# Optimization experiments

Hardware: AMD Instinct MI355X
Metric: run time of the kernel (lower is better)

## Reference

```python
import jax, jax.numpy as jnp
import numpy as np

EPS = 1e-5

def _ln(x, g=None, b=None):
    m = x.mean(-1, keepdims=True)
    v = x.var(-1, keepdims=True)
    y = (x - m) / jnp.sqrt(v + EPS)
    if g is not None:
        y = y * g + b
    return y

def setup_inputs() -> dict:
    B, N, D, E, NC = 32, 256, 1024, 4096, 16
    key = jax.random.key(0)
    ks = iter(jax.random.split(key, 24))
    def rn(shape, s=0.02):
        return jax.random.normal(next(ks), shape, jnp.float32) * s
    return dict(
        h=jax.random.normal(next(ks), (B, N, D), jnp.float32),
        Wpp=rn((D, E)), bpp=jnp.zeros(E), Wsp=rn((D, E)), bsp=jnp.zeros(E),
        Wq=rn((E, E)), bq=jnp.zeros(E),
        Wk=rn((E, E)), bk=jnp.zeros(E),
        Wv=rn((E, E)), bv=jnp.zeros(E),
        g_pfs=jnp.ones(D + E), b_pfs=jnp.zeros(D + E),
        Wpfs=rn((D + E, D)), bpfs=jnp.zeros(D),
        g_sfs=jnp.ones(E), b_sfs=jnp.zeros(E),
        Wsfs=rn((E, D)), bsfs=jnp.zeros(D),
        Wpc=rn((D, NC)), bpc=jnp.zeros(NC),
        Wc0=rn((NC, 8, D)), bc0=jnp.zeros((NC, 8)),
        Wc1=rn((NC, 16, D)), bc1=jnp.zeros((NC, 16)),
        Wc2=rn((NC, 32, D)), bc2=jnp.zeros((NC, 32)),
    )

def reference(h, Wpp, bpp, Wsp, bsp, Wq, bq, Wk, bk, Wv, bv,
              g_pfs, b_pfs, Wpfs, bpfs, g_sfs, b_sfs, Wsfs, bsfs,
              Wpc, bpc, Wc0, bc0, Wc1, bc1, Wc2, bc2):
    B, N, D = h.shape
    H = 4
    E = Wpp.shape[1]
    hd = E // H
    scale = hd ** -0.5
    gelu = lambda x: jax.nn.gelu(x, approximate=False)  # torch exact GELU
    pp = gelu(h @ Wpp + bpp)                  # [B,N,E]
    sp = gelu(h @ Wsp + bsp)                  # [B,N,E]
    Q = (pp @ Wq + bq).reshape(B, N, H, hd)
    K = (sp @ Wk + bk).reshape(B, N, H, hd)
    V = (sp @ Wv + bv).reshape(B, N, H, hd)
    attn = jax.nn.softmax(jnp.einsum('bqhd,bkhd->bhqk', Q, K) * scale, axis=-1)
    intf = jnp.einsum('bhqk,bkhd->bqhd', attn, V).reshape(B, N, E)
    intf = _ln(intf)                          # F.layer_norm, no affine
    pvec = _ln((_ln(jnp.concatenate([h, intf], -1), g_pfs, b_pfs) @ Wpfs + bpfs).mean(1))  # [B,D]
    svec = _ln((_ln(sp, g_sfs, b_sfs) @ Wsfs + bsfs).mean(1))                               # [B,D]
    parent_logits = pvec @ Wpc + bpc          # [B,NC]
    y_hat = jnp.argmax(parent_logits, axis=1) # argmax(softmax) == argmax(logits)
    # routed child heads: gather per-sample weight by parent argmax, batched matvec
    child = tuple(
        jnp.einsum('bd,bnd->bn', svec, W[y_hat]) + b[y_hat]
        for W, b in ((Wc0, bc0), (Wc1, bc1), (Wc2, bc2))
    )
    return (parent_logits,) + child + (pvec, svec)
```

## Files before the change

### kernel.cpp

```cpp
#include <hip/hip_runtime.h>
#include <hip/hip_bf16.h>

typedef __bf16 bf16x8 __attribute__((ext_vector_type(8)));
typedef float f32x4 __attribute__((ext_vector_type(4)));
typedef unsigned long long u64;

#define EPSV 1e-5f

__device__ __forceinline__ float bf2f(unsigned short u){
  unsigned int x = ((unsigned int)u) << 16;
  return __builtin_bit_cast(float, x);
}
__device__ __forceinline__ unsigned short f2bf(float f){
  __bf16 b = (__bf16)f;
  return __builtin_bit_cast(unsigned short, b);
}
__device__ __forceinline__ float gelu_exact(float x){
  return 0.5f * x * (1.0f + erff(x * 0.7071067811865476f));
}
__device__ __forceinline__ void gload_lds16(const void* g, void* l){
  __builtin_amdgcn_global_load_lds((const __attribute__((address_space(1))) unsigned int*)g,
                                   (__attribute__((address_space(3))) unsigned int*)l, 16, 0, 0);
}

struct GemmCore {
  char* smem; int t, w, l, wm, wn, lr, lg, bm0, bn0, nk;
  int srow, sslot;
  const unsigned short *A, *B; int lda, ldb;
  f32x4 acc[8][4];
  bf16x8 a0[4][2], a1[4][2], b0[2][2], b1[2][2];

  __device__ __forceinline__ void stage(int kt, int mat, int hf, int q){
    if (kt >= nk) return;
    const int r_h = q*64 + srow;
    const int s_ = sslot ^ ((r_h >> 1) & 7);
    const unsigned short* gp = (mat ? B + (size_t)(bn0 + hf*128 + r_h)*ldb
                                    : A + (size_t)(bm0 + hf*128 + r_h)*lda)
                               + (kt << 6) + s_*8;
    char* lp = smem + mat*65536 + (kt&1)*32768 + hf*16384 + q*8192 + t*16;
    gload_lds16((const void*)gp, (void*)lp);
  }
  __device__ __forceinline__ bf16x8 rdA(int d, int fm, int kk){
    const int r = fm*16 + lr;
    const int s_ = (kk*4 + lg) ^ ((r >> 1) & 7);
    return *(const bf16x8*)(smem + d*32768 + wm*16384 + r*128 + s_*16);
  }
  __device__ __forceinline__ bf16x8 rdB(int d, int fn, int kk){
    const int r = (wn&1)*64 + fn*16 + lr;
    const int s_ = (kk*4 + lg) ^ ((r >> 1) & 7);
    return *(const bf16x8*)(smem + 65536 + d*32768 + (wn>>1)*16384 + r*128 + s_*16);
  }
  __device__ __forceinline__ void ktile(int kt, int d){
    stage(kt+1, 0, 0, 1); stage(kt+1, 0, 1, 1);
    #pragma unroll
    for (int fm=0; fm<4; ++fm){ a0[fm][0] = rdA(d, fm, 0); a0[fm][1] = rdA(d, fm, 1); }
    #pragma unroll
    for (int fn=0; fn<2; ++fn){ b0[fn][0] = rdB(d, fn, 0); b0[fn][1] = rdB(d, fn, 1); }
    __builtin_amdgcn_s_barrier();
    __builtin_amdgcn_s_setprio(1);
    #pragma unroll
    for (int fm=0; fm<4; ++fm)
      #pragma unroll
      for (int fn=0; fn<2; ++fn)
        #pragma unroll
        for (int kk=0; kk<2; ++kk)
          acc[fm][fn] = __builtin_amdgcn_mfma_f32_16x16x32_bf16(a0[fm][kk], b0[fn][kk], acc[fm][fn], 0,0,0);
    __builtin_amdgcn_s_setprio(0);
    #pragma unroll
    for (int fn=0; fn<2; ++fn){ b1[fn][0] = rdB(d, fn+2, 0); b1[fn][1] = rdB(d, fn+2, 1); }
    __builtin_amdgcn_s_barrier();
    __builtin_amdgcn_s_setprio(1);
    #pragma unroll
    for (int fm=0; fm<4; ++fm)
      #pragma unroll
      for (int fn=0; fn<2; ++fn)
        #pragma unroll
        for (int kk=0; kk<2; ++kk)
          acc[fm][fn+2] = __builtin_amdgcn_mfma_f32_16x16x32_bf16(a0[fm][kk], b1[fn][kk], acc[fm][fn+2], 0,0,0);
    __builtin_amdgcn_s_setprio(0);
    stage(kt+2, 0, 0, 0); stage(kt+2, 0, 1, 0);
    stage(kt+2, 1, 0, 0); stage(kt+2, 1, 1, 0);
    #pragma unroll
    for (int fm=0; fm<4; ++fm){ a1[fm][0] = rdA(d, fm+4, 0); a1[fm][1] = rdA(d, fm+4, 1); }
    __builtin_amdgcn_s_barrier();
    __builtin_amdgcn_s_setprio(1);
    #pragma unroll
    for (int fm=0; fm<4; ++fm)
      #pragma unroll
      for (int fn=0; fn<2; ++fn)
        #pragma unroll
        for (int kk=0; kk<2; ++kk)
          acc[fm+4][fn+2] = __builtin_amdgcn_mfma_f32_16x16x32_bf16(a1[fm][kk], b1[fn][kk], acc[fm+4][fn+2], 0,0,0);
    __builtin_amdgcn_s_setprio(0);
    stage(kt+2, 1, 0, 1); stage(kt+2, 1, 1, 1);
    __builtin_amdgcn_s_barrier();
    __builtin_amdgcn_s_setprio(1);
    #pragma unroll
    for (int fm=0; fm<4; ++fm)
      #pragma unroll
      for (int fn=0; fn<2; ++fn)
        #pragma unroll
        for (int kk=0; kk<2; ++kk)
          acc[fm+4][fn] = __builtin_amdgcn_mfma_f32_16x16x32_bf16(a1[fm][kk], b0[fn][kk], acc[fm+4][fn], 0,0,0);
    __builtin_amdgcn_s_setprio(0);
    if (kt + 2 < nk) { asm volatile("s_waitcnt vmcnt(6)" ::: "memory"); }
    else             { asm volatile("s_waitcnt vmcnt(0)" ::: "memory"); }
  }
  __device__ __forceinline__ void run(){
    #pragma unroll
    for (int i=0;i<8;++i)
      #pragma unroll
      for (int j=0;j<4;++j){ f32x4 zz = {0.f,0.f,0.f,0.f}; acc[i][j] = zz; }
    stage(0,0,0,0); stage(0,0,1,0); stage(0,0,0,1); stage(0,0,1,1);
    stage(0,1,0,0); stage(0,1,1,0); stage(0,1,0,1); stage(0,1,1,1);
    stage(1,0,0,0); stage(1,0,1,0);
    stage(1,1,0,0); stage(1,1,1,0);
    stage(1,1,0,1); stage(1,1,1,1);
    asm volatile("s_waitcnt vmcnt(6)" ::: "memory");
    __builtin_amdgcn_s_barrier();
    for (int kt = 0; kt < nk; kt += 2){ ktile(kt, 0); ktile(kt+1, 1); }
  }
  __device__ __forceinline__ void init(char* sm, int Kd, const unsigned short* A_,
                                       const unsigned short* B_, int lda_, int ldb_,
                                       int bm0_, int bn0_){
    smem = sm; t = threadIdx.x; w = t>>6; l = t&63;
    wm = w>>2; wn = w&3; lr = l&15; lg = l>>4;
    srow = t>>3; sslot = t&7;
    A = A_; B = B_; lda = lda_; ldb = ldb_; bm0 = bm0_; bn0 = bn0_;
    nk = Kd >> 6;
  }
};

template<int MODE>
__global__ __launch_bounds__(512, 2)
void gemm256(const unsigned short* __restrict__ A, const unsigned short* __restrict__ B,
             const float* __restrict__ bias0, const float* __restrict__ bias1,
             void* __restrict__ C0v, void* __restrict__ C1v,
             int Kd, int lda, int ldb, int ldc)
{
  __shared__ char smem[131072];
  const int nbx = gridDim.x;
  const int nwg = nbx * gridDim.y;
  int bid = blockIdx.y*nbx + blockIdx.x;
  if ((nwg & 7) == 0) bid = (bid & 7)*(nwg >> 3) + (bid >> 3);
  GemmCore g;
  g.init(smem, Kd, A, B, lda, ldb, (bid / nbx) * 256, (bid % nbx) * 256);
  g.run();
  #pragma unroll
  for (int fm=0; fm<8; ++fm){
    #pragma unroll
    for (int fn=0; fn<4; ++fn){
      const int row0 = g.bm0 + g.wm*128 + fm*16 + g.lg*4;
      const int col  = g.bn0 + g.wn*64 + fn*16 + g.lr;
      f32x4 v = g.acc[fm][fn];
      if constexpr (MODE == 3){
        unsigned short* C = (unsigned short*)C0v;
        const float bb = bias0[col];
        u64 pack = 0;
        #pragma unroll
        for (int j=0;j<4;++j) pack |= (u64)f2bf(v[j] + bb) << (16*j);
        *(u64*)(C + (size_t)col*256 + (size_t)(row0>>8)*1048576 + (row0&255)) = pack;
      } else {
        const bool hi = (MODE == 0) && (col >= 4096);
        unsigned short* C = (unsigned short*)(hi ? C1v : C0v);
        const int c2 = hi ? (col - 4096) : col;
        const float bb = hi ? bias1[c2] : bias0[c2];
        #pragma unroll
        for (int j=0;j<4;++j){
          float x = v[j] + bb;
          if constexpr (MODE==0) x = gelu_exact(x);
          C[(size_t)(row0+j)*ldc + c2] = f2bf(x);
        }
      }
    }
  }
}

__global__ __launch_bounds__(512, 2)
void gemm_qkv(const unsigned short* __restrict__ App, const unsigned short* __restrict__ Asp,
              const unsigned short* __restrict__ Wqkv,
              const float* __restrict__ bq, const float* __restrict__ bk,
              const float* __restrict__ bv,
              unsigned short* __restrict__ Qo, unsigned short* __restrict__ Ko,
              unsigned short* __restrict__ Vto)
{
  __shared__ char smem[131072];
  const int z = blockIdx.z;
  const int nbx = gridDim.x;
  const int nwg = nbx * gridDim.y;
  int bid = blockIdx.y*nbx + blockIdx.x;
  if ((nwg & 7) == 0) bid = (bid & 7)*(nwg >> 3) + (bid >> 3);
  GemmCore g;
  g.init(smem, 4096, (z==0) ? App : Asp, Wqkv + (size_t)z*16777216, 4096, 4096,
         (bid / nbx) * 256, (bid % nbx) * 256);
  g.run();
  const float* bias = (z==0) ? bq : (z==1) ? bk : bv;
  #pragma unroll
  for (int fm=0; fm<8; ++fm){
    #pragma unroll
    for (int fn=0; fn<4; ++fn){
      const int row0 = g.bm0 + g.wm*128 + fm*16 + g.lg*4;
      const int col  = g.bn0 + g.wn*64 + fn*16 + g.lr;
      f32x4 v = g.acc[fm][fn];
      const float bb = bias[col];
      if (z == 2){
        u64 pack = 0;
        #pragma unroll
        for (int j=0;j<4;++j) pack |= (u64)f2bf(v[j] + bb) << (16*j);
        *(u64*)(Vto + (size_t)col*256 + (size_t)(row0>>8)*1048576 + (row0&255)) = pack;
      } else {
        unsigned short* C = (z==0) ? Qo : Ko;
        #pragma unroll
        for (int j=0;j<4;++j) C[(size_t)(row0+j)*4096 + col] = f2bf(v[j] + bb);
      }
    }
  }
}

template<int MODE>
__global__ __launch_bounds__(256)
void gemm_bt(const unsigned short* __restrict__ A, const unsigned short* __restrict__ B,
             const float* __restrict__ bias, void* __restrict__ Cv,
             int Kd, int lda, int ldb, int ldc,
             long sA2, long sA1, long sB2, long sB1, long sC2, long sC1,
             float scale)
{
  __shared__ unsigned short lds[2][2][4096];
  const int t = threadIdx.x;
  const int w = t >> 6, l = t & 63;
  const int z = blockIdx.z;
  A += (size_t)(z>>2)*sA2 + (size_t)(z&3)*sA1;
  B += (size_t)(z>>2)*sB2 + (size_t)(z&3)*sB1;
  const int bm0 = blockIdx.y * 128, bn0 = blockIdx.x * 128;
  const int nk = Kd >> 5;

  const int sr = l >> 2;
  const int ss = l & 3;

  f32x4 acc[4][4];
  #pragma unroll
  for (int i=0;i<4;++i){
    #pragma unroll
    for (int j=0;j<4;++j){ f32x4 zz = {0.f,0.f,0.f,0.f}; acc[i][j] = zz; }
  }

  const int wm = w >> 1, wn = w & 1;
  const int lr = l & 15, lg = l >> 4;

  auto stage = [&](int kt, int bb){
    const int k0 = kt << 5;
    #pragma unroll
    for (int i=0;i<2;++i){
      const int r  = w*32 + i*16 + sr;
      const int sa = ss ^ ((r>>1)&3);
      const unsigned short* ga = A + (size_t)(bm0 + r)*lda + (k0 + sa*8);
      gload_lds16((const void*)ga, (void*)((char*)&lds[bb][0][0] + w*2048 + i*1024));
      const unsigned short* gb = B + (size_t)(bn0 + r)*ldb + (k0 + sa*8);
      gload_lds16((const void*)gb, (void*)((char*)&lds[bb][1][0] + w*2048 + i*1024));
    }
  };

  int buf = 0;
  stage(0, 0);
  for (int kt=0; kt<nk; ++kt){
    __syncthreads();
    if (kt+1 < nk) stage(kt+1, buf^1);
    bf16x8 av[4], bv[4];
    #pragma unroll
    for (int fm=0; fm<4; ++fm){
      const int row = wm*64 + fm*16 + lr;
      const int sl  = lg ^ ((row>>1)&3);
      av[fm] = *(const bf16x8*)((const char*)&lds[buf][0][0] + row*64 + sl*16);
    }
    #pragma unroll
    for (int fn=0; fn<4; ++fn){
      const int col = wn*64 + fn*16 + lr;
      const int sl  = lg ^ ((col>>1)&3);
      bv[fn] = *(const bf16x8*)((const char*)&lds[buf][1][0] + col*64 + sl*16);
    }
    #pragma unroll
    for (int fm=0; fm<4; ++fm){
      #pragma unroll
      for (int fn=0; fn<4; ++fn)
        acc[fm][fn] = __builtin_amdgcn_mfma_f32_16x16x32_bf16(av[fm], bv[fn], acc[fm][fn], 0,0,0);
    }
    buf ^= 1;
  }

  const size_t coff = (size_t)(z>>2)*sC2 + (size_t)(z&3)*sC1;
  #pragma unroll
  for (int fm=0; fm<4; ++fm){
    #pragma unroll
    for (int fn=0; fn<4; ++fn){
      const int row0 = bm0 + wm*64 + fm*16 + lg*4;
      const int col  = bn0 + wn*64 + fn*16 + lr;
      f32x4 v = acc[fm][fn];
      if constexpr (MODE == 2){
        float* C = (float*)Cv + coff;
        #pragma unroll
        for (int j=0;j<4;++j) C[(size_t)(row0+j)*ldc + col] = v[j]*scale;
      }
    }
  }
}

__global__ __launch_bounds__(256)
void k_convh(const float* __restrict__ in, unsigned short* __restrict__ out){
  const size_t id = (size_t)blockIdx.x*256 + threadIdx.x;
  float4 v = ((const float4*)in)[id];
  u64 pack = (u64)f2bf(v.x) | ((u64)f2bf(v.y)<<16) | ((u64)f2bf(v.z)<<32) | ((u64)f2bf(v.w)<<48);
  *(u64*)(out + id*4) = pack;
}

__global__ __launch_bounds__(256)
void k_tconv3(const float* __restrict__ W0, const float* __restrict__ W1,
              const float* __restrict__ W2, unsigned short* __restrict__ Wt,
              int Kd, int N, long wtStride){
  __shared__ float lt[64][65];
  const int t = threadIdx.x;
  const int zz = blockIdx.z;
  const float* W = (zz==0) ? W0 : (zz==1) ? W1 : W2;
  unsigned short* Wtz = Wt + (size_t)zz * wtStride;
  const int n0 = blockIdx.x*64, k0 = blockIdx.y*64;
  #pragma unroll
  for (int i=0;i<16;++i){
    int lin = i*256 + t; int r = lin>>6, c = lin&63;
    lt[r][c] = W[(size_t)(k0+r)*N + n0 + c];
  }
  __syncthreads();
  #pragma unroll
  for (int i=0;i<16;++i){
    int lin = i*256 + t; int n = lin>>6, k = lin&63;
    Wtz[(size_t)(n0+n)*Kd + k0 + k] = f2bf(lt[k][n]);
  }
}

__global__ __launch_bounds__(256)
void k_tconv(const float* __restrict__ W, unsigned short* __restrict__ Wt, int Kd, int N){
  __shared__ float lt[64][65];
  const int t = threadIdx.x;
  const int n0 = blockIdx.x*64, k0 = blockIdx.y*64;
  #pragma unroll
  for (int i=0;i<16;++i){
    int lin = i*256 + t; int r = lin>>6, c = lin&63;
    lt[r][c] = W[(size_t)(k0+r)*N + n0 + c];
  }
  __syncthreads();
  #pragma unroll
  for (int i=0;i<16;++i){
    int lin = i*256 + t; int n = lin>>6, k = lin&63;
    Wt[(size_t)(n0+n)*Kd + k0 + k] = f2bf(lt[k][n]);
  }
}

__global__ __launch_bounds__(256)
void k_softmax(const float* __restrict__ S, unsigned short* __restrict__ P){
  const int t = threadIdx.x, w = t>>6, l = t&63;
  const size_t row = (size_t)blockIdx.x*4 + w;
  float4 v = *(const float4*)(S + row*256 + l*4);
  float m = fmaxf(fmaxf(v.x,v.y), fmaxf(v.z,v.w));
  #pragma unroll
  for (int off=32; off; off>>=1) m = fmaxf(m, __shfl_xor(m, off));
  float e0 = expf(v.x-m), e1 = expf(v.y-m), e2 = expf(v.z-m), e3 = expf(v.w-m);
  float s = e0+e1+e2+e3;
  #pragma unroll
  for (int off=32; off; off>>=1) s += __shfl_xor(s, off);
  const float inv = 1.0f/s;
  u64 pack = (u64)f2bf(e0*inv) | ((u64)f2bf(e1*inv)<<16) | ((u64)f2bf(e2*inv)<<32) | ((u64)f2bf(e3*inv)<<48);
  *(u64*)(P + row*256 + l*4) = pack;
}

__device__ __forceinline__ void blkred2(float& a, float& b, float* sred, int t){
  #pragma unroll
  for (int off=32; off; off>>=1){ a += __shfl_xor(a, off); b += __shfl_xor(b, off); }
  __syncthreads();
  if ((t&63)==0){ sred[(t>>6)*2] = a; sred[(t>>6)*2+1] = b; }
  __syncthreads();
  a = sred[0]+sred[2]+sred[4]+sred[6];
  b = sred[1]+sred[3]+sred[5]+sred[7];
}

__device__ __forceinline__ void blkred4(float& a, float& b, float& c, float& d,
                                        float* sred, int t){
  #pragma unroll
  for (int off=32; off; off>>=1){
    a += __shfl_xor(a, off); b += __shfl_xor(b, off);
    c += __shfl_xor(c, off); d += __shfl_xor(d, off);
  }
  __syncthreads();
  if ((t&63)==0){
    sred[(t>>6)*4]   = a; sred[(t>>6)*4+1] = b;
    sred[(t>>6)*4+2] = c; sred[(t>>6)*4+3] = d;
  }
  __syncthreads();
  a = sred[0]+sred[4]+sred[8]+sred[12];
  b = sred[1]+sred[5]+sred[9]+sred[13];
  c = sred[2]+sred[6]+sred[10]+sred[14];
  d = sred[3]+sred[7]+sred[11]+sred[15];
}

__global__ __launch_bounds__(256)
void k_stats(const float* __restrict__ h, const float* __restrict__ intf,
             const unsigned short* __restrict__ sp,
             const float* __restrict__ g_pfs, const float* __restrict__ b_pfs,
             const float* __restrict__ g_sfs, const float* __restrict__ b_sfs,
             float* __restrict__ part_p, float* __restrict__ part_s, int g0)
{
  __shared__ float sred[16];
  const int bl = blockIdx.x, grp = blockIdx.y, t = threadIdx.x;
  float zacc[20], wacc[16];
  #pragma unroll
  for (int j=0;j<20;++j) zacc[j]=0.f;
  #pragma unroll
  for (int j=0;j<16;++j) wacc[j]=0.f;
  for (int rr=0; rr<16; ++rr){
    const size_t r = (size_t)bl*256 + grp*16 + rr;
    float hv[4], iv[16], sv[16];
    #pragma unroll
    for (int j=0;j<4;++j) hv[j] = h[r*1024 + j*256 + t];
    float s1=0.f, s2=0.f;
    #pragma unroll
    for (int j=0;j<16;++j){ float x = intf[r*4096 + j*256 + t]; iv[j]=x; s1+=x; s2+=x*x; }
    float u1=0.f, u2=0.f;
    #pragma unroll
    for (int j=0;j<16;++j){ float x = bf2f(sp[r*4096 + j*256 + t]); sv[j]=x; u1+=x; u2+=x*x; }
    blkred4(s1,s2,u1,u2,sred,t);
    const float m1 = s1*(1.f/4096.f);
    const float rs1 = rsqrtf(fmaxf(s2*(1.f/4096.f) - m1*m1, 0.f) + EPSV);
    const float m3 = u1*(1.f/4096.f);
    const float rs3 = rsqrtf(fmaxf(u2*(1.f/4096.f) - m3*m3, 0.f) + EPSV);
    #pragma unroll
    for (int j=0;j<16;++j){ int idx = j*256+t; wacc[j] += ((sv[j]-m3)*rs3)*g_sfs[idx] + b_sfs[idx]; }
    float t1=0.f, t2=0.f;
    #pragma unroll
    for (int j=0;j<4;++j){ t1 += hv[j]; t2 += hv[j]*hv[j]; }
    #pragma unroll
    for (int j=0;j<16;++j){ float y = (iv[j]-m1)*rs1; iv[j]=y; t1+=y; t2+=y*y; }
    blkred2(t1,t2,sred,t);
    const float m2 = t1*(1.f/5120.f);
    const float rs2 = rsqrtf(fmaxf(t2*(1.f/5120.f) - m2*m2, 0.f) + EPSV);
    #pragma unroll
    for (int j=0;j<4;++j){ int idx = j*256+t; zacc[j] += ((hv[j]-m2)*rs2)*g_pfs[idx] + b_pfs[idx]; }
    #pragma unroll
    for (int j=0;j<16;++j){ int idx = 1024 + j*256+t; zacc[4+j] += ((iv[j]-m2)*rs2)*g_pfs[idx] + b_pfs[idx]; }
  }
  const size_t pb = (size_t)(g0 + bl)*16 + grp;
  #pragma unroll
  for (int j=0;j<20;++j) part_p[pb*5120 + j*256 + t] = zacc[j];
  #pragma unroll
  for (int j=0;j<16;++j) part_s[pb*4096 + j*256 + t] = wacc[j];
}

__global__ __launch_bounds__(256)
void k_reduce(const float* __restrict__ part_p, const float* __restrict__ part_s,
              float* __restrict__ xbar, float* __restrict__ ybar){
  int id = blockIdx.x*256 + threadIdx.x;
  if (id < 32*5120){
    const int b = id / 5120, i = id % 5120;
    float s = 0.f;
    for (int g=0; g<16; ++g) s += part_p[((size_t)b*16+g)*5120 + i];
    xbar[(size_t)b*5120 + i] = s * (1.f/256.f);
  } else {
    id -= 32*5120;
    const int b = id / 4096, i = id % 4096;
    float s = 0.f;
    for (int g=0; g<16; ++g) s += part_s[((size_t)b*16+g)*4096 + i];
    ybar[(size_t)b*4096 + i] = s * (1.f/256.f);
  }
}

__global__ __launch_bounds__(256)
void k_proj_part(const float* __restrict__ xbar, const float* __restrict__ ybar,
                 const float* __restrict__ Wpfs, const float* __restrict__ Wsfs,
                 float* __restrict__ pbuf){
  const int path = blockIdx.z;
  const int y = blockIdx.y;
  if (path == 1 && y >= 8) return;
  const int Kp = path ? 4096 : 5120;
  const float* X = path ? ybar : xbar;
  const float* W = path ? Wsfs : Wpfs;
  const int t = threadIdx.x;
  const int col = blockIdx.x*64 + (t & 63);
  const int sub = t >> 6;
  const int k0 = y*512 + sub*128;
  float acc[32];
  #pragma unroll
  for (int b=0;b<32;++b) acc[b] = 0.f;
  for (int i4=0; i4<32; ++i4){
    const int k = k0 + i4*4;
    float wv0 = W[(size_t)(k  )*1024 + col];
    float wv1 = W[(size_t)(k+1)*1024 + col];
    float wv2 = W[(size_t)(k+2)*1024 + col];
    float wv3 = W[(size_t)(k+3)*1024 + col];
    #pragma unroll
    for (int b=0;b<32;++b){
      float4 xv = *(const float4*)(X + (size_t)b*Kp + k);
      acc[b] += xv.x*wv0 + xv.y*wv1 + xv.z*wv2 + xv.w*wv3;
    }
  }
  float* dst = pbuf + ((size_t)(path*40 + y*4 + sub)*32)*1024 + col;
  #pragma unroll
  for (int b=0;b<32;++b) dst[(size_t)b*1024] = acc[b];
}

__global__ __launch_bounds__(256)
void k_projred(const float* __restrict__ pbuf,
               const float* __restrict__ bpfs, const float* __restrict__ bsfs,
               float* __restrict__ tpre, float* __restrict__ spre){
  const int id = blockIdx.x*256 + threadIdx.x;
  const int path = id >> 15;
  const int rem = id & 32767;
  const int b = rem >> 10, col = rem & 1023;
  const int ns = path ? 32 : 40;
  const float* src = pbuf + ((size_t)(path*40)*32 + b)*1024 + col;
  float s = path ? bsfs[col] : bpfs[col];
  for (int g=0; g<ns; ++g) s += src[(size_t)g*32*1024];
  (path ? spre : tpre)[(size_t)b*1024 + col] = s;
}

__global__ __launch_bounds__(256)
void k_lnrow(const float* __restrict__ tpre, const float* __restrict__ spre,
             float* __restrict__ out){
  __shared__ float sred[16];
  const int id = blockIdx.x, t = threadIdx.x;
  const int path = id >> 5, b = id & 31;
  const float* src = (path ? spre : tpre) + (size_t)b*1024;
  float v[4]; float s1=0.f, s2=0.f;
  #pragma unroll
  for (int j=0;j<4;++j){ v[j] = src[j*256+t]; s1 += v[j]; s2 += v[j]*v[j]; }
  blkred2(s1,s2,sred,t);
  const float m = s1*(1.f/1024.f);
  const float rs = rsqrtf(fmaxf(s2*(1.f/1024.f)-m*m,0.f)+EPSV);
  float* dst = out + (path ? 35072 : 2304) + (size_t)b*1024;
  #pragma unroll
  for (int j=0;j<4;++j) dst[j*256+t] = (v[j]-m)*rs;
}

__global__ __launch_bounds__(256)
void k_head(const float* __restrict__ Wpc, const float* __restrict__ bpc,
            const float* __restrict__ Wc0, const float* __restrict__ bc0,
            const float* __restrict__ Wc1, const float* __restrict__ bc1,
            const float* __restrict__ Wc2, const float* __restrict__ bc2,
            float* __restrict__ out){
  __shared__ float slog[16];
  __shared__ int sy;
  const int b = blockIdx.x, t = threadIdx.x, w = t>>6, l = t&63;
  const float* pv = out + 2304 + (size_t)b*1024;
  const float* sv = out + 35072 + (size_t)b*1024;
  #pragma unroll
  for (int jj=0; jj<4; ++jj){
    const int j = w*4 + jj;
    float a = 0.f;
    for (int i=l; i<1024; i+=64) a += pv[i]*Wpc[(size_t)i*16 + j];
    #pragma unroll
    for (int off=32; off; off>>=1) a += __shfl_xor(a, off);
    if (l==0){ const float lgv = a + bpc[j]; slog[j] = lgv; out[b*16 + j] = lgv; }
  }
  __syncthreads();
  if (t==0){
    int best=0; float bvv = slog[0];
    for (int i=1;i<16;++i) if (slog[i] > bvv){ bvv = slog[i]; best = i; }
    sy = best;
  }
  __syncthreads();
  const int y = sy;
  const float* Ws[3] = {Wc0, Wc1, Wc2};
  const float* bs[3] = {bc0, bc1, bc2};
  const int nouts[3] = {8,16,32};
  const int ooff[3]  = {512, 768, 1280};
  for (int hI=0; hI<3; ++hI){
    const int no = nouts[hI];
    for (int n = w; n < no; n += 4){
      const float* wr = Ws[hI] + ((size_t)y*no + n)*1024;
      float a = 0.f;
      for (int i=l; i<1024; i+=64) a += sv[i]*wr[i];
      #pragma unroll
      for (int off=32; off; off>>=1) a += __shfl_xor(a, off);
      if (l==0) out[ooff[hI] + b*no + n] = a + bs[hI][(size_t)y*no + n];
    }
  }
}

extern "C" void kernel_launch(void* const* d_in, const int* in_sizes, int n_in,
                              void* d_out, int out_size, void* d_ws, size_t ws_size,
                              hipStream_t stream)
{
  const float* h    = (const float*)d_in[0];
  const float* Wpp  = (const float*)d_in[1];
  const float* bpp  = (const float*)d_in[2];
  const float* Wsp  = (const float*)d_in[3];
  const float* bsp  = (const float*)d_in[4];
  const float* Wq   = (const float*)d_in[5];
  const float* bq   = (const float*)d_in[6];
  const float* Wk   = (const float*)d_in[7];
  const float* bk   = (const float*)d_in[8];
  const float* Wv   = (const float*)d_in[9];
  const float* bv   = (const float*)d_in[10];
  const float* g_pfs= (const float*)d_in[11];
  const float* b_pfs= (const float*)d_in[12];
  const float* Wpfs = (const float*)d_in[13];
  const float* bpfs = (const float*)d_in[14];
  const float* g_sfs= (const float*)d_in[15];
  const float* b_sfs= (const float*)d_in[16];
  const float* Wsfs = (const float*)d_in[17];
  const float* bsfs = (const float*)d_in[18];
  const float* Wpc  = (const float*)d_in[19];
  const float* bpc  = (const float*)d_in[20];
  const float* Wc0  = (const float*)d_in[21];
  const float* bc0  = (const float*)d_in[22];
  const float* Wc1  = (const float*)d_in[23];
  const float* bc1  = (const float*)d_in[24];
  const float* Wc2  = (const float*)d_in[25];
  const float* bc2  = (const float*)d_in[26];
  float* out = (float*)d_out;
  char* ws = (char*)d_ws;
  (void)in_sizes; (void)n_in; (void)out_size;

  struct PlanT { int G, NS, hoist; };
  const PlanT plans[8] = {{16,4096,2},{16,4096,1},{16,4096,0},{8,4096,0},{4,4096,0},{2,4096,0},{1,4096,0},{1,1024,0}};
  int G = 0, NS = 0, HOIST = 0;
  size_t oWt=0,oWps=0,oWq=0,oSP=0;
  size_t oPp=0,oPs=0,oXb=0,oYb=0,oTp=0,oSp=0,oPbf=0,oHb=0,oPb=0,oSb=0,oQ=0,oK=0,oVt=0;
  for (int pi = 0; pi < 8; ++pi){
    const size_t g = plans[pi].G, ns = plans[pi].NS;
    const int hoist = plans[pi].hoist;
    size_t off = 0;
    auto alloc = [&](size_t bytes){ size_t o = off; off += (bytes + 255) & ~255ULL; return o; };
    size_t wt=0, wps=0, wq=0, sp2=0, pbf=0, hb=0, pb=0;
    size_t pp_, ps_, xb, yb, tp, sp_, sb, q, k, vt;
    if (hoist >= 1){
      wps = alloc(8192ULL*1024*2);
      wq  = alloc(3*4096ULL*4096*2);
      pp_ = alloc(32ULL*16*5120*4);
      ps_ = alloc(32ULL*16*4096*4);
      xb = alloc(32*5120*4); yb = alloc(32*4096*4);
      tp = alloc(32*1024*4); sp_ = alloc(32*1024*4);
      sb = alloc(g*2097152);
      q  = alloc(g*2097152);
      k  = alloc(g*2097152);
      vt = alloc(g*2097152);
      if (hoist == 2){
        sp2 = alloc(g*2097152);
        pb = sp2;
      } else {
        sp2 = alloc(g*1572864);
        pb = k;
      }
      pbf = q; hb = vt;
    } else {
      wt = alloc(ns*4096*2);
      pp_ = alloc(32ULL*16*5120*4);
      ps_ = alloc(32ULL*16*4096*4);
      xb = alloc(32*5120*4); yb = alloc(32*4096*4);
      tp = alloc(32*1024*4); sp_ = alloc(32*1024*4);
      pbf = alloc(2*40*32*1024*4);
      hb = alloc(g*524288);
      pb = alloc(g*2097152);
      sb = alloc(g*2097152);
      q  = alloc(g*2097152);
      k  = alloc(g*2097152);
      vt = alloc(g*2097152);
      sp2 = pb;
    }
    if (off <= ws_size){
      G = (int)g; NS = (int)ns; HOIST = hoist;
      oWt=wt; oWps=wps; oWq=wq; oSP=sp2;
      oPp=pp_; oPs=ps_; oXb=xb; oYb=yb; oTp=tp; oSp=sp_; oPbf=pbf;
      oHb=hb; oPb=pb; oSb=sb; oQ=q; oK=k; oVt=vt;
      break;
    }
  }
  if (!G) return;

  unsigned short* Wt    = (unsigned short*)(ws + oWt);
  unsigned short* WpsT  = (unsigned short*)(ws + oWps);
  unsigned short* WqkvT = (unsigned short*)(ws + oWq);
  float* part_p = (float*)(ws + oPp);
  float* part_s = (float*)(ws + oPs);
  float* xbar   = (float*)(ws + oXb);
  float* ybar   = (float*)(ws + oYb);
  float* tpre   = (float*)(ws + oTp);
  float* spre   = (float*)(ws + oSp);
  float* pbuf   = (float*)(ws + oPbf);
  unsigned short* h_bf = (unsigned short*)(ws + oHb);
  unsigned short* pp   = (unsigned short*)(ws + oPb);
  unsigned short* sp   = (unsigned short*)(ws + oSb);
  unsigned short* Q    = (unsigned short*)(ws + oQ);
  unsigned short* Kb   = (unsigned short*)(ws + oK);
  unsigned short* Vt   = (unsigned short*)(ws + oVt);
  float*          S    = (float*)(ws + oSP);
  unsigned short* P    = (unsigned short*)(ws + oSP + (size_t)G*1048576);
  float*          intf = (float*)(ws + oQ);

  const float scale = 1.0f/32.0f;
  (void)oK;

  if (HOIST >= 1){
    hipLaunchKernelGGL(k_tconv, dim3(64,16), dim3(256), 0, stream, Wpp, WpsT, 1024, 4096);
    hipLaunchKernelGGL(k_tconv, dim3(64,16), dim3(256), 0, stream, Wsp, WpsT + 4096ULL*1024, 1024, 4096);
    hipLaunchKernelGGL(k_tconv3, dim3(64,64,3), dim3(256), 0, stream,
                       Wq, Wk, Wv, WqkvT, 4096, 4096, 16777216L);
  }

  for (int g0 = 0; g0 < 32; g0 += G){
    const float* h_g = h + (size_t)g0*262144;

    hipLaunchKernelGGL(k_convh, dim3(G*256), dim3(256), 0, stream, h_g, h_bf);

    if (HOIST == 2){
      hipLaunchKernelGGL(gemm256<0>, dim3(32,G), dim3(512), 0, stream,
                         h_bf, WpsT, bpp, bsp, (void*)pp, (void*)sp, 1024, 1024,1024,4096);
      hipLaunchKernelGGL(gemm_qkv, dim3(16,G,3), dim3(512), 0, stream,
                         pp, sp, WqkvT, bq, bk, bv, Q, Kb, Vt);
    } else if (HOIST == 1){
      hipLaunchKernelGGL(gemm256<0>, dim3(32,G), dim3(512), 0, stream,
                         h_bf, WpsT, bpp, bsp, (void*)pp, (void*)sp, 1024, 1024,1024,4096);
      hipLaunchKernelGGL(gemm256<1>, dim3(16,G), dim3(512), 0, stream,
                         pp, WqkvT, bq, bq, (void*)Q, (void*)Q, 4096, 4096,4096,4096);
      hipLaunchKernelGGL(gemm256<1>, dim3(16,G), dim3(512), 0, stream,
                         sp, WqkvT + 16777216ULL, bk, bk, (void*)Kb, (void*)Kb, 4096, 4096,4096,4096);
      hipLaunchKernelGGL(gemm256<3>, dim3(16,G), dim3(512), 0, stream,
                         sp, WqkvT + 33554432ULL, bv, bv, (void*)Vt, (void*)Vt, 4096, 4096,4096,256);
    } else {
      hipLaunchKernelGGL(k_tconv, dim3(64,16), dim3(256), 0, stream, Wpp, Wt, 1024, 4096);
      hipLaunchKernelGGL(gemm256<0>, dim3(16,G), dim3(512), 0, stream,
                         h_bf, Wt, bpp, bpp, (void*)pp, (void*)pp, 1024, 1024,1024,4096);
      for (int nso = 0; nso < 4096; nso += NS){
        hipLaunchKernelGGL(k_tconv, dim3(NS/64,64), dim3(256), 0, stream, Wq + nso, Wt, 4096, 4096);
        hipLaunchKernelGGL(gemm256<1>, dim3(NS/256,G), dim3(512), 0, stream,
                           pp, Wt, bq + nso, bq + nso, (void*)(Q + nso), (void*)(Q + nso), 4096, 4096,4096,4096);
      }
      hipLaunchKernelGGL(k_tconv, dim3(64,16), dim3(256), 0, stream, Wsp, Wt, 1024, 4096);
      hipLaunchKernelGGL(gemm256<0>, dim3(16,G), dim3(512), 0, stream,
                         h_bf, Wt, bsp, bsp, (void*)sp, (void*)sp, 1024, 1024,1024,4096);
      for (int nso = 0; nso < 4096; nso += NS){
        hipLaunchKernelGGL(k_tconv, dim3(NS/64,64), dim3(256), 0, stream, Wk + nso, Wt, 4096, 4096);
        hipLaunchKernelGGL(gemm256<1>, dim3(NS/256,G), dim3(512), 0, stream,
                           sp, Wt, bk + nso, bk + nso, (void*)(Kb + nso), (void*)(Kb + nso), 4096, 4096,4096,4096);
      }
      for (int nso = 0; nso < 4096; nso += NS){
        hipLaunchKernelGGL(k_tconv, dim3(NS/64,64), dim3(256), 0, stream, Wv + nso, Wt, 4096, 4096);
        hipLaunchKernelGGL(gemm256<3>, dim3(NS/256,G), dim3(512), 0, stream,
                           sp, Wt, bv + nso, bv + nso, (void*)(Vt + (size_t)nso*256), (void*)(Vt + (size_t)nso*256), 4096, 4096,4096,256);
      }
    }
    hipLaunchKernelGGL(gemm_bt<2>, dim3(2,2,G*4), dim3(256), 0, stream,
                       Q, Kb, (const float*)nullptr, (void*)S, 1024, 4096,4096,256,
                       1048576L,1024L, 1048576L,1024L, 262144L,65536L, scale);
    hipLaunchKernelGGL(k_softmax, dim3(G*256), dim3(256), 0, stream, S, P);
    hipLaunchKernelGGL(gemm_bt<2>, dim3(8,2,G*4), dim3(256), 0, stream,
                       P, Vt, (const float*)nullptr, (void*)intf, 256, 256,256,4096,
                       262144L,65536L, 1048576L,262144L, 1048576L,1024L, 1.f);
    hipLaunchKernelGGL(k_stats, dim3(G,16), dim3(256), 0, stream,
                       h_g, intf, sp, g_pfs, b_pfs, g_sfs, b_sfs, part_p, part_s, g0);
  }

  hipLaunchKernelGGL(k_reduce, dim3(1152), dim3(256), 0, stream, part_p, part_s, xbar, ybar);
  hipLaunchKernelGGL(k_proj_part, dim3(16,10,2), dim3(256), 0, stream,
                     xbar, ybar, Wpfs, Wsfs, pbuf);
  hipLaunchKernelGGL(k_projred, dim3(256), dim3(256), 0, stream,
                     pbuf, bpfs, bsfs, tpre, spre);
  hipLaunchKernelGGL(k_lnrow, dim3(64), dim3(256), 0, stream, tpre, spre, out);
  hipLaunchKernelGGL(k_head, dim3(32), dim3(256), 0, stream,
                     Wpc, bpc, Wc0, bc0, Wc1, bc1, Wc2, bc2, out);
}
```

Baseline: 1.281 ms.

## Add aliased single-pass workspace plan and store attention output in bf16

Adds a primary path that processes the whole batch at once using a compact workspace. Buffers are aliased between stages (pp/Vt, Q/intf, h_bf/Kb/pbuf, S/part_p) and one transposed weight buffer is reused for Wq, Wk and Wv, so the grouped loop and its extra launches go away when the workspace fits. The attention-output GEMM now writes intf as bf16 (new MODE 5) and k_stats reads it as bf16, which halves that traffic but lowers the precision of the layer-norm input. The fallback plan list is reduced and the weight-streaming variants are removed.

```diff
diff --git a/kernel.cpp b/kernel.cpp
--- a/kernel.cpp
+++ b/kernel.cpp
@@ -299,6 +299,10 @@
         float* C = (float*)Cv + coff;
         #pragma unroll
         for (int j=0;j<4;++j) C[(size_t)(row0+j)*ldc + col] = v[j]*scale;
+      } else if constexpr (MODE == 5){
+        unsigned short* C = (unsigned short*)Cv + coff;
+        #pragma unroll
+        for (int j=0;j<4;++j) C[(size_t)(row0+j)*ldc + col] = f2bf(v[j]*scale);
       }
     }
   }
@@ -310,6 +314,24 @@
   float4 v = ((const float4*)in)[id];
   u64 pack = (u64)f2bf(v.x) | ((u64)f2bf(v.y)<<16) | ((u64)f2bf(v.z)<<32) | ((u64)f2bf(v.w)<<48);
   *(u64*)(out + id*4) = pack;
+}
+
+__global__ __launch_bounds__(256)
+void k_tconv(const float* __restrict__ W, unsigned short* __restrict__ Wt, int Kd, int N){
+  __shared__ float lt[64][65];
+  const int t = threadIdx.x;
+  const int n0 = blockIdx.x*64, k0 = blockIdx.y*64;
+  #pragma unroll
+  for (int i=0;i<16;++i){
+    int lin = i*256 + t; int r = lin>>6, c = lin&63;
+    lt[r][c] = W[(size_t)(k0+r)*N + n0 + c];
+  }
+  __syncthreads();
+  #pragma unroll
+  for (int i=0;i<16;++i){
+    int lin = i*256 + t; int n = lin>>6, k = lin&63;
+    Wt[(size_t)(n0+n)*Kd + k0 + k] = f2bf(lt[k][n]);
+  }
 }
 
 __global__ __launch_bounds__(256)
@@ -336,24 +358,6 @@
 }
 
 __global__ __launch_bounds__(256)
-void k_tconv(const float* __restrict__ W, unsigned short* __restrict__ Wt, int Kd, int N){
-  __shared__ float lt[64][65];
-  const int t = threadIdx.x;
-  const int n0 = blockIdx.x*64, k0 = blockIdx.y*64;
-  #pragma unroll
-  for (int i=0;i<16;++i){
-    int lin = i*256 + t; int r = lin>>6, c = lin&63;
-    lt[r][c] = W[(size_t)(k0+r)*N + n0 + c];
-  }
-  __syncthreads();
-  #pragma unroll
-  for (int i=0;i<16;++i){
-    int lin = i*256 + t; int n = lin>>6, k = lin&63;
-    Wt[(size_t)(n0+n)*Kd + k0 + k] = f2bf(lt[k][n]);
-  }
-}
-
-__global__ __launch_bounds__(256)
 void k_softmax(const float* __restrict__ S, unsigned short* __restrict__ P){
   const int t = threadIdx.x, w = t>>6, l = t&63;
   const size_t row = (size_t)blockIdx.x*4 + w;
@@ -400,7 +404,7 @@
 }
 
 __global__ __launch_bounds__(256)
-void k_stats(const float* __restrict__ h, const float* __restrict__ intf,
+void k_stats(const float* __restrict__ h, const unsigned short* __restrict__ intf,
              const unsigned short* __restrict__ sp,
              const float* __restrict__ g_pfs, const float* __restrict__ b_pfs,
              const float* __restrict__ g_sfs, const float* __restrict__ b_sfs,
@@ -420,7 +424,7 @@
     for (int j=0;j<4;++j) hv[j] = h[r*1024 + j*256 + t];
     float s1=0.f, s2=0.f;
     #pragma unroll
-    for (int j=0;j<16;++j){ float x = intf[r*4096 + j*256 + t]; iv[j]=x; s1+=x; s2+=x*x; }
+    for (int j=0;j<16;++j){ float x = bf2f(intf[r*4096 + j*256 + t]); iv[j]=x; s1+=x; s2+=x*x; }
     float u1=0.f, u2=0.f;
     #pragma unroll
     for (int j=0;j<16;++j){ float x = bf2f(sp[r*4096 + j*256 + t]); sv[j]=x; u1+=x; u2+=x*x; }
@@ -616,63 +620,109 @@
   char* ws = (char*)d_ws;
   (void)in_sizes; (void)n_in; (void)out_size;
 
-  struct PlanT { int G, NS, hoist; };
-  const PlanT plans[8] = {{16,4096,2},{16,4096,1},{16,4096,0},{8,4096,0},{4,4096,0},{2,4096,0},{1,4096,0},{1,1024,0}};
-  int G = 0, NS = 0, HOIST = 0;
-  size_t oWt=0,oWps=0,oWq=0,oSP=0;
+  const float scale = 1.0f/32.0f;
+
+  {
+    size_t off = 0;
+    auto alloc = [&](size_t bytes){ size_t o = off; off += (bytes + 255) & ~255ULL; return o; };
+    size_t oWps = alloc(8192ULL*1024*2);
+    size_t oWb  = alloc(4096ULL*4096*2);
+    size_t oA   = alloc(64ULL<<20);
+    size_t oB   = alloc(64ULL<<20);
+    size_t oC   = alloc(64ULL<<20);
+    size_t oD   = alloc(64ULL<<20);
+    size_t oXb  = alloc(32*5120*4);
+    size_t oYb  = alloc(32*4096*4);
+    size_t oTp  = alloc(32*1024*4);
+    size_t oSp  = alloc(32*1024*4);
+    if (off <= ws_size){
+      unsigned short* WpsT = (unsigned short*)(ws + oWps);
+      unsigned short* wbuf = (unsigned short*)(ws + oWb);
+      unsigned short* pp   = (unsigned short*)(ws + oA);
+      unsigned short* Vt   = (unsigned short*)(ws + oA);
+      unsigned short* sp   = (unsigned short*)(ws + oB);
+      unsigned short* Q    = (unsigned short*)(ws + oC);
+      unsigned short* intf = (unsigned short*)(ws + oC);
+      unsigned short* h_bf = (unsigned short*)(ws + oD);
+      unsigned short* Kb   = (unsigned short*)(ws + oD);
+      float* pbuf   = (float*)(ws + oD);
+      float* S      = (float*)(ws + oWb);
+      unsigned short* P = (unsigned short*)(ws + oWps);
+      float* part_p = (float*)(ws + oWb);
+      float* part_s = (float*)(ws + oWb + ((32ULL*16*5120*4 + 255) & ~255ULL));
+      float* xbar   = (float*)(ws + oXb);
+      float* ybar   = (float*)(ws + oYb);
+      float* tpre   = (float*)(ws + oTp);
+      float* spre   = (float*)(ws + oSp);
+
+      hipLaunchKernelGGL(k_tconv, dim3(64,16), dim3(256), 0, stream, Wpp, WpsT, 1024, 4096);
+      hipLaunchKernelGGL(k_tconv, dim3(64,16), dim3(256), 0, stream, Wsp, WpsT + 4096ULL*1024, 1024, 4096);
+      hipLaunchKernelGGL(k_convh, dim3(8192), dim3(256), 0, stream, h, h_bf);
+      hipLaunchKernelGGL(gemm256<0>, dim3(32,32), dim3(512), 0, stream,
+                         h_bf, WpsT, bpp, bsp, (void*)pp, (void*)sp, 1024, 1024,1024,4096);
+      hipLaunchKernelGGL(k_tconv, dim3(64,64), dim3(256), 0, stream, Wq, wbuf, 4096, 4096);
+      hipLaunchKernelGGL(gemm256<1>, dim3(16,32), dim3(512), 0, stream,
+                         pp, wbuf, bq, bq, (void*)Q, (void*)Q, 4096, 4096,4096,4096);
+      hipLaunchKernelGGL(k_tconv, dim3(64,64), dim3(256), 0, stream, Wk, wbuf, 4096, 4096);
+      hipLaunchKernelGGL(gemm256<1>, dim3(16,32), dim3(512), 0, stream,
+                         sp, wbuf, bk, bk, (void*)Kb, (void*)Kb, 4096, 4096,4096,4096);
+      hipLaunchKernelGGL(k_tconv, dim3(64,64), dim3(256), 0, stream, Wv, wbuf, 4096, 4096);
+      hipLaunchKernelGGL(gemm256<3>, dim3(16,32), dim3(512), 0, stream,
+                         sp, wbuf, bv, bv, (void*)Vt, (void*)Vt, 4096, 4096,4096,256);
+      hipLaunchKernelGGL(gemm_bt<2>, dim3(2,2,128), dim3(256), 0, stream,
+                         Q, Kb, (const float*)nullptr, (void*)S, 1024, 4096,4096,256,
+                         1048576L,1024L, 1048576L,1024L, 262144L,65536L, scale);
+      hipLaunchKernelGGL(k_softmax, dim3(8192), dim3(256), 0, stream, S, P);
+      hipLaunchKernelGGL(gemm_bt<5>, dim3(8,2,128), dim3(256), 0, stream,
+                         P, Vt, (const float*)nullptr, (void*)intf, 256, 256,256,4096,
+                         262144L,65536L, 1048576L,262144L, 1048576L,1024L, 1.f);
+      hipLaunchKernelGGL(k_stats, dim3(32,16), dim3(256), 0, stream,
+                         h, intf, sp, g_pfs, b_pfs, g_sfs, b_sfs, part_p, part_s, 0);
+      hipLaunchKernelGGL(k_reduce, dim3(1152), dim3(256), 0, stream, part_p, part_s, xbar, ybar);
+      hipLaunchKernelGGL(k_proj_part, dim3(16,10,2), dim3(256), 0, stream,
+                         xbar, ybar, Wpfs, Wsfs, pbuf);
+      hipLaunchKernelGGL(k_projred, dim3(256), dim3(256), 0, stream,
+                         pbuf, bpfs, bsfs, tpre, spre);
+      hipLaunchKernelGGL(k_lnrow, dim3(64), dim3(256), 0, stream, tpre, spre, out);
+      hipLaunchKernelGGL(k_head, dim3(32), dim3(256), 0, stream,
+                         Wpc, bpc, Wc0, bc0, Wc1, bc1, Wc2, bc2, out);
+      return;
+    }
+  }
+
+  struct PlanT { int G, hoist; };
+  const PlanT plans[3] = {{16,2},{16,1},{8,1}};
+  int G = 0, HOIST = 0;
+  size_t oWps=0,oWq=0,oSP=0;
   size_t oPp=0,oPs=0,oXb=0,oYb=0,oTp=0,oSp=0,oPbf=0,oHb=0,oPb=0,oSb=0,oQ=0,oK=0,oVt=0;
-  for (int pi = 0; pi < 8; ++pi){
-    const size_t g = plans[pi].G, ns = plans[pi].NS;
+  for (int pi = 0; pi < 3; ++pi){
+    const size_t g = plans[pi].G;
     const int hoist = plans[pi].hoist;
     size_t off = 0;
     auto alloc = [&](size_t bytes){ size_t o = off; off += (bytes + 255) & ~255ULL; return o; };
-    size_t wt=0, wps=0, wq=0, sp2=0, pbf=0, hb=0, pb=0;
-    size_t pp_, ps_, xb, yb, tp, sp_, sb, q, k, vt;
-    if (hoist >= 1){
-      wps = alloc(8192ULL*1024*2);
-      wq  = alloc(3*4096ULL*4096*2);
-      pp_ = alloc(32ULL*16*5120*4);
-      ps_ = alloc(32ULL*16*4096*4);
-      xb = alloc(32*5120*4); yb = alloc(32*4096*4);
-      tp = alloc(32*1024*4); sp_ = alloc(32*1024*4);
-      sb = alloc(g*2097152);
-      q  = alloc(g*2097152);
-      k  = alloc(g*2097152);
-      vt = alloc(g*2097152);
-      if (hoist == 2){
-        sp2 = alloc(g*2097152);
-        pb = sp2;
-      } else {
-        sp2 = alloc(g*1572864);
-        pb = k;
-      }
-      pbf = q; hb = vt;
-    } else {
-      wt = alloc(ns*4096*2);
-      pp_ = alloc(32ULL*16*5120*4);
-      ps_ = alloc(32ULL*16*4096*4);
-      xb = alloc(32*5120*4); yb = alloc(32*4096*4);
-      tp = alloc(32*1024*4); sp_ = alloc(32*1024*4);
-      pbf = alloc(2*40*32*1024*4);
-      hb = alloc(g*524288);
-      pb = alloc(g*2097152);
-      sb = alloc(g*2097152);
-      q  = alloc(g*2097152);
-      k  = alloc(g*2097152);
-      vt = alloc(g*2097152);
-      sp2 = pb;
-    }
+    size_t wps = alloc(8192ULL*1024*2);
+    size_t wq  = alloc(3*4096ULL*4096*2);
+    size_t pp_ = alloc(32ULL*16*5120*4);
+    size_t ps_ = alloc(32ULL*16*4096*4);
+    size_t xb = alloc(32*5120*4); size_t yb = alloc(32*4096*4);
+    size_t tp = alloc(32*1024*4); size_t sp_ = alloc(32*1024*4);
+    size_t sb = alloc(g*2097152);
+    size_t q  = alloc(g*2097152);
+    size_t k  = alloc(g*2097152);
+    size_t vt = alloc(g*2097152);
+    size_t sp2, pb;
+    if (hoist == 2){ sp2 = alloc(g*2097152); pb = sp2; }
+    else           { sp2 = alloc(g*1572864); pb = k; }
     if (off <= ws_size){
-      G = (int)g; NS = (int)ns; HOIST = hoist;
-      oWt=wt; oWps=wps; oWq=wq; oSP=sp2;
-      oPp=pp_; oPs=ps_; oXb=xb; oYb=yb; oTp=tp; oSp=sp_; oPbf=pbf;
-      oHb=hb; oPb=pb; oSb=sb; oQ=q; oK=k; oVt=vt;
+      G = (int)g; HOIST = hoist;
+      oWps=wps; oWq=wq; oSP=sp2;
+      oPp=pp_; oPs=ps_; oXb=xb; oYb=yb; oTp=tp; oSp=sp_; oPbf=q;
+      oHb=vt; oPb=pb; oSb=sb; oQ=q; oK=k; oVt=vt;
       break;
     }
   }
   if (!G) return;
 
-  unsigned short* Wt    = (unsigned short*)(ws + oWt);
   unsigned short* WpsT  = (unsigned short*)(ws + oWps);
   unsigned short* WqkvT = (unsigned short*)(ws + oWq);
   float* part_p = (float*)(ws + oPp);
@@ -690,65 +740,34 @@
   unsigned short* Vt   = (unsigned short*)(ws + oVt);
   float*          S    = (float*)(ws + oSP);
   unsigned short* P    = (unsigned short*)(ws + oSP + (size_t)G*1048576);
-  float*          intf = (float*)(ws + oQ);
-
-  const float scale = 1.0f/32.0f;
-  (void)oK;
-
-  if (HOIST >= 1){
-    hipLaunchKernelGGL(k_tconv, dim3(64,16), dim3(256), 0, stream, Wpp, WpsT, 1024, 4096);
-    hipLaunchKernelGGL(k_tconv, dim3(64,16), dim3(256), 0, stream, Wsp, WpsT + 4096ULL*1024, 1024, 4096);
-    hipLaunchKernelGGL(k_tconv3, dim3(64,64,3), dim3(256), 0, stream,
-                       Wq, Wk, Wv, WqkvT, 4096, 4096, 16777216L);
-  }
+  unsigned short* intf = (unsigned short*)(ws + oQ);
+
+  hipLaunchKernelGGL(k_tconv, dim3(64,16), dim3(256), 0, stream, Wpp, WpsT, 1024, 4096);
+  hipLaunchKernelGGL(k_tconv, dim3(64,16), dim3(256), 0, stream, Wsp, WpsT + 4096ULL*1024, 1024, 4096);
+  hipLaunchKernelGGL(k_tconv3, dim3(64,64,3), dim3(256), 0, stream,
+                     Wq, Wk, Wv, WqkvT, 4096, 4096, 16777216L);
 
   for (int g0 = 0; g0 < 32; g0 += G){
     const float* h_g = h + (size_t)g0*262144;
-
     hipLaunchKernelGGL(k_convh, dim3(G*256), dim3(256), 0, stream, h_g, h_bf);
-
+    hipLaunchKernelGGL(gemm256<0>, dim3(32,G), dim3(512), 0, stream,
+                       h_bf, WpsT, bpp, bsp, (void*)pp, (void*)sp, 1024, 1024,1024,4096);
     if (HOIST == 2){
-      hipLaunchKernelGGL(gemm256<0>, dim3(32,G), dim3(512), 0, stream,
-                         h_bf, WpsT, bpp, bsp, (void*)pp, (void*)sp, 1024, 1024,1024,4096);
       hipLaunchKernelGGL(gemm_qkv, dim3(16,G,3), dim3(512), 0, stream,
                          pp, sp, WqkvT, bq, bk, bv, Q, Kb, Vt);
-    } else if (HOIST == 1){
-      hipLaunchKernelGGL(gemm256<0>, dim3(32,G), dim3(512), 0, stream,
-                         h_bf, WpsT, bpp, bsp, (void*)pp, (void*)sp, 1024, 1024,1024,4096);
+    } else {
       hipLaunchKernelGGL(gemm256<1>, dim3(16,G), dim3(512), 0, stream,
                          pp, WqkvT, bq, bq, (void*)Q, (void*)Q, 4096, 4096,4096,4096);
       hipLaunchKernelGGL(gemm256<1>, dim3(16,G), dim3(512), 0, stream,
                          sp, WqkvT + 16777216ULL, bk, bk, (void*)Kb, (void*)Kb, 4096, 4096,4096,4096);
       hipLaunchKernelGGL(gemm256<3>, dim3(16,G), dim3(512), 0, stream,
                          sp, WqkvT + 33554432ULL, bv, bv, (void*)Vt, (void*)Vt, 4096, 4096,4096,256);
-    } else {
-      hipLaunchKernelGGL(k_tconv, dim3(64,16), dim3(256), 0, stream, Wpp, Wt, 1024, 4096);
-      hipLaunchKernelGGL(gemm256<0>, dim3(16,G), dim3(512), 0, stream,
-                         h_bf, Wt, bpp, bpp, (void*)pp, (void*)pp, 1024, 1024,1024,4096);
-      for (int nso = 0; nso < 4096; nso += NS){
-        hipLaunchKernelGGL(k_tconv, dim3(NS/64,64), dim3(256), 0, stream, Wq + nso, Wt, 4096, 4096);
-        hipLaunchKernelGGL(gemm256<1>, dim3(NS/256,G), dim3(512), 0, stream,
-                           pp, Wt, bq + nso, bq + nso, (void*)(Q + nso), (void*)(Q + nso), 4096, 4096,4096,4096);
-      }
-      hipLaunchKernelGGL(k_tconv, dim3(64,16), dim3(256), 0, stream, Wsp, Wt, 1024, 4096);
-      hipLaunchKernelGGL(gemm256<0>, dim3(16,G), dim3(512), 0, stream,
-                         h_bf, Wt, bsp, bsp, (void*)sp, (void*)sp, 1024, 1024,1024,4096);
-      for (int nso = 0; nso < 4096; nso += NS){
-        hipLaunchKernelGGL(k_tconv, dim3(NS/64,64), dim3(256), 0, stream, Wk + nso, Wt, 4096, 4096);
-        hipLaunchKernelGGL(gemm256<1>, dim3(NS/256,G), dim3(512), 0, stream,
-                           sp, Wt, bk + nso, bk + nso, (void*)(Kb + nso), (void*)(Kb + nso), 4096, 4096,4096,4096);
-      }
-      for (int nso = 0; nso < 4096; nso += NS){
-        hipLaunchKernelGGL(k_tconv, dim3(NS/64,64), dim3(256), 0, stream, Wv + nso, Wt, 4096, 4096);
-        hipLaunchKernelGGL(gemm256<3>, dim3(NS/256,G), dim3(512), 0, stream,
-                           sp, Wt, bv + nso, bv + nso, (void*)(Vt + (size_t)nso*256), (void*)(Vt + (size_t)nso*256), 4096, 4096,4096,256);
-      }
     }
     hipLaunchKernelGGL(gemm_bt<2>, dim3(2,2,G*4), dim3(256), 0, stream,
                        Q, Kb, (const float*)nullptr, (void*)S, 1024, 4096,4096,256,
                        1048576L,1024L, 1048576L,1024L, 262144L,65536L, scale);
     hipLaunchKernelGGL(k_softmax, dim3(G*256), dim3(256), 0, stream, S, P);
-    hipLaunchKernelGGL(gemm_bt<2>, dim3(8,2,G*4), dim3(256), 0, stream,
+    hipLaunchKernelGGL(gemm_bt<5>, dim3(8,2,G*4), dim3(256), 0, stream,
                        P, Vt, (const float*)nullptr, (void*)intf, 256, 256,256,4096,
                        262144L,65536L, 1048576L,262144L, 1048576L,1024L, 1.f);
     hipLaunchKernelGGL(k_stats, dim3(G,16), dim3(256), 0, stream,
```

New measurement: 1.277 ms. No clear change (-0.3%).
